# Kernel optimization log

Measured on AMD Instinct MI355X. Metric: run time of the kernel, lower is better.

## Reference

```python
import jax, jax.numpy as jnp
import numpy as np


def _minmax_norm(m):
    # per-sample min-max normalize over all non-batch dims (channel=1, h, w)
    mn = m.min(axis=(1, 2, 3), keepdims=True)
    mx = m.max(axis=(1, 2, 3), keepdims=True)
    return (m - mn) / (mx - mn)


def setup_inputs() -> dict:
    key = jax.random.key(0)
    k1, k2, k3, k4, k5 = jax.random.split(key, 5)
    N, C, H, W = 32, 256, 56, 56
    Ce, He, We = 512, 14, 14
    return {
        "main_inputs": jax.random.normal(k1, (N, C, H, W), dtype=jnp.float32),
        "embedding_inputs": jax.random.normal(k2, (N, Ce, He, We), dtype=jnp.float32),
        "conv_w": jax.random.normal(k3, (C, Ce), dtype=jnp.float32) * (1.0 / np.sqrt(Ce)),
        "conv_b": jax.random.normal(k4, (C,), dtype=jnp.float32) * 0.01,
        "weight": jax.random.normal(k5, (), dtype=jnp.float32),
    }


def reference(main_inputs, embedding_inputs, conv_w, conv_b, weight):
    N, C, H, W = main_inputs.shape
    Ce = embedding_inputs.shape[1]
    # nn.Upsample(size=(H,W), mode='bilinear', align_corners=False) == half-pixel linear resize
    up = jax.image.resize(embedding_inputs, (N, Ce, H, W), method="linear")  # [N,Ce,H,W]
    # 1x1 conv Ce -> C
    emb = jnp.einsum("nchw,oc->nohw", up, conv_w) + conv_b[None, :, None, None]  # [N,C,H,W]
    # reshape_and_normalize_masks(squeeze=True): mean over channels, per-sample min-max
    mask = emb.mean(axis=1, keepdims=True)  # [N,1,H,W]
    mask = _minmax_norm(mask)
    # second call with squeeze=False (inference_x is None): normalize again
    mask = _minmax_norm(mask)
    s = jax.nn.sigmoid(main_inputs)
    return s * mask * weight + s
```

## Files before the change

### kernel.cpp

```cpp
#include <hip/hip_runtime.h>
#include <math.h>

#define W_PART_OFF 0
#define WSUM_OFF   32768
#define P2_OFF     33280
#define MASK_OFF   83456

__global__ void k_wsum_part(const float* __restrict__ conv_w, float* __restrict__ ws) {
    int b = blockIdx.x;
    int t = threadIdx.x;
    float a0 = 0.f, a1 = 0.f;
    int o0 = b * 4;
#pragma unroll
    for (int o = o0; o < o0 + 4; ++o) {
        a0 += conv_w[o * 512 + t];
        a1 += conv_w[o * 512 + t + 256];
    }
    ws[W_PART_OFF + b * 512 + t]       = a0;
    ws[W_PART_OFF + b * 512 + t + 256] = a1;
}

__global__ void k_wsum_final(float* __restrict__ ws) {
    int c = blockIdx.x * 256 + threadIdx.x;
    float a = 0.f;
#pragma unroll 8
    for (int k = 0; k < 64; ++k) a += ws[W_PART_OFF + k * 512 + c];
    ws[WSUM_OFF + c] = a;
}

__global__ void k_mask_small(const float* __restrict__ emb, float* __restrict__ ws) {
    __shared__ float wl[64];
    int n  = blockIdx.x;
    int cc = blockIdx.y;
    int t  = threadIdx.x;
    if (t < 64) wl[t] = ws[WSUM_OFF + cc * 64 + t];
    __syncthreads();
    if (t < 196) {
        const float* base = emb + (size_t)(n * 512 + cc * 64) * 196 + t;
        float acc = 0.f;
#pragma unroll 8
        for (int c = 0; c < 64; ++c) acc += base[c * 196] * wl[c];
        ws[P2_OFF + (n * 8 + cc) * 196 + t] = acc;
    }
}

__global__ void k_upsample(const float* __restrict__ wgt_p, float* __restrict__ ws) {
    __shared__ float sm[196];
    __shared__ float rmin[256], rmax[256];
    int n = blockIdx.x;
    int t = threadIdx.x;

    if (t < 196) {
        float a = 0.f;
#pragma unroll
        for (int k = 0; k < 8; ++k) a += ws[P2_OFF + (n * 8 + k) * 196 + t];
        sm[t] = a;
    }
    __syncthreads();

    float vmin = INFINITY, vmax = -INFINITY;
    for (int p = t; p < 3136; p += 256) {
        int h = p / 56, w = p % 56;
        float sy = (h + 0.5f) * 0.25f - 0.5f;
        float sx = (w + 0.5f) * 0.25f - 0.5f;
        int y0 = (int)floorf(sy); float fy = sy - (float)y0;
        int x0 = (int)floorf(sx); float fx = sx - (float)x0;
        int y1 = min(y0 + 1, 13); y0 = max(y0, 0);
        int x1 = min(x0 + 1, 13); x0 = max(x0, 0);
        float v00 = sm[y0 * 14 + x0], v01 = sm[y0 * 14 + x1];
        float v10 = sm[y1 * 14 + x0], v11 = sm[y1 * 14 + x1];
        float v = (1.f - fy) * ((1.f - fx) * v00 + fx * v01)
                +        fy  * ((1.f - fx) * v10 + fx * v11);
        vmin = fminf(vmin, v);
        vmax = fmaxf(vmax, v);
    }
    rmin[t] = vmin; rmax[t] = vmax;
    __syncthreads();
    for (int s = 128; s > 0; s >>= 1) {
        if (t < s) {
            rmin[t] = fminf(rmin[t], rmin[t + s]);
            rmax[t] = fmaxf(rmax[t], rmax[t + s]);
        }
        __syncthreads();
    }
    float mn = rmin[0], mx = rmax[0];
    float a = wgt_p[0] / (mx - mn);
    float b = 1.f - mn * a;

    for (int p = t; p < 3136; p += 256) {
        int h = p / 56, w = p % 56;
        float sy = (h + 0.5f) * 0.25f - 0.5f;
        float sx = (w + 0.5f) * 0.25f - 0.5f;
        int y0 = (int)floorf(sy); float fy = sy - (float)y0;
        int x0 = (int)floorf(sx); float fx = sx - (float)x0;
        int y1 = min(y0 + 1, 13); y0 = max(y0, 0);
        int x1 = min(x0 + 1, 13); x0 = max(x0, 0);
        float v00 = sm[y0 * 14 + x0], v01 = sm[y0 * 14 + x1];
        float v10 = sm[y1 * 14 + x0], v11 = sm[y1 * 14 + x1];
        float v = (1.f - fy) * ((1.f - fx) * v00 + fx * v01)
                +        fy  * ((1.f - fx) * v10 + fx * v11);
        ws[MASK_OFF + n * 3136 + p] = v * a + b;
    }
}

__global__ void __launch_bounds__(256) k_final(const float4* __restrict__ x4,
                                               const float* __restrict__ ws,
                                               float4* __restrict__ out4) {
    const float4* m4 = (const float4*)(ws + MASK_OFF);
    const int total4 = 6422528;
    int stride = gridDim.x * blockDim.x;
    for (int g = blockIdx.x * blockDim.x + threadIdx.x; g < total4; g += stride) {
        int n  = g / 200704;
        int p4 = g % 784;
        float4 m = m4[n * 784 + p4];
        float4 x = x4[g];
        float4 o;
        o.x = m.x * __builtin_amdgcn_rcpf(1.f + __expf(-x.x));
        o.y = m.y * __builtin_amdgcn_rcpf(1.f + __expf(-x.y));
        o.z = m.z * __builtin_amdgcn_rcpf(1.f + __expf(-x.z));
        o.w = m.w * __builtin_amdgcn_rcpf(1.f + __expf(-x.w));
        out4[g] = o;
    }
}

extern "C" void kernel_launch(void* const* d_in, const int* in_sizes, int n_in,
                              void* d_out, int out_size, void* d_ws, size_t ws_size,
                              hipStream_t stream) {
    const float* main_in = (const float*)d_in[0];
    const float* emb_in  = (const float*)d_in[1];
    const float* conv_w  = (const float*)d_in[2];
    const float* weight  = (const float*)d_in[4];

    float* ws  = (float*)d_ws;
    float4* out = (float4*)d_out;

    k_wsum_part <<<64,            256, 0, stream>>>(conv_w, ws);
    k_wsum_final<<<2,             256, 0, stream>>>(ws);
    k_mask_small<<<dim3(32, 8),   256, 0, stream>>>(emb_in, ws);
    k_upsample  <<<32,            256, 0, stream>>>(weight, ws);
    k_final     <<<2048,          256, 0, stream>>>((const float4*)main_in, ws, out);
}
```

Measured before the change: 56.50 us.

## Restructure final kernel with per-sample LDS mask and nontemporal stores

The final elementwise kernel drops the grid-stride loop for a fixed mapping in which each block handles 4096 float4s of one sample. That sample's mask is staged once in shared memory, and the per-element divide/modulo indexing is replaced by an incrementally wrapped index. Outputs are written with nontemporal stores so the streamed output does not pollute cache. The cost is a shared-memory fill plus a barrier per block, and a grid size hard-coded to the problem shape.

```diff
diff --git a/kernel.cpp b/kernel.cpp
--- a/kernel.cpp
+++ b/kernel.cpp
@@ -1,5 +1,7 @@
 #include <hip/hip_runtime.h>
 #include <math.h>
+
+typedef float vfloat4 __attribute__((ext_vector_type(4)));
 
 #define W_PART_OFF 0
 #define WSUM_OFF   32768
@@ -106,20 +108,32 @@
 __global__ void __launch_bounds__(256) k_final(const float4* __restrict__ x4,
                                                const float* __restrict__ ws,
                                                float4* __restrict__ out4) {
-    const float4* m4 = (const float4*)(ws + MASK_OFF);
-    const int total4 = 6422528;
-    int stride = gridDim.x * blockDim.x;
-    for (int g = blockIdx.x * blockDim.x + threadIdx.x; g < total4; g += stride) {
-        int n  = g / 200704;
-        int p4 = g % 784;
-        float4 m = m4[n * 784 + p4];
-        float4 x = x4[g];
-        float4 o;
+    __shared__ float4 mlds[784];
+    const int bid = blockIdx.x;
+    const int t   = threadIdx.x;
+    const int n   = bid / 49;
+    const int s   = bid - n * 49;
+    const float4* m4 = (const float4*)(ws + MASK_OFF) + n * 784;
+    for (int k = t; k < 784; k += 256) mlds[k] = m4[k];
+    __syncthreads();
+
+    const long base = (long)n * 200704 + (long)s * 4096;
+    const float4* xp = x4 + base;
+    vfloat4*      op = (vfloat4*)(out4 + base);
+    int p = (s * 176 + t) % 784;
+
+#pragma unroll 8
+    for (int i = 0; i < 16; ++i) {
+        float4 x = xp[i * 256 + t];
+        float4 m = mlds[p];
+        vfloat4 o;
         o.x = m.x * __builtin_amdgcn_rcpf(1.f + __expf(-x.x));
         o.y = m.y * __builtin_amdgcn_rcpf(1.f + __expf(-x.y));
         o.z = m.z * __builtin_amdgcn_rcpf(1.f + __expf(-x.z));
         o.w = m.w * __builtin_amdgcn_rcpf(1.f + __expf(-x.w));
-        out4[g] = o;
+        __builtin_nontemporal_store(o, &op[i * 256 + t]);
+        p += 256;
+        if (p >= 784) p -= 784;
     }
 }
 
@@ -131,12 +145,12 @@
     const float* conv_w  = (const float*)d_in[2];
     const float* weight  = (const float*)d_in[4];
 
-    float* ws  = (float*)d_ws;
+    float* ws   = (float*)d_ws;
     float4* out = (float4*)d_out;
 
-    k_wsum_part <<<64,            256, 0, stream>>>(conv_w, ws);
-    k_wsum_final<<<2,             256, 0, stream>>>(ws);
-    k_mask_small<<<dim3(32, 8),   256, 0, stream>>>(emb_in, ws);
-    k_upsample  <<<32,            256, 0, stream>>>(weight, ws);
-    k_final     <<<2048,          256, 0, stream>>>((const float4*)main_in, ws, out);
+    k_wsum_part <<<64,          256, 0, stream>>>(conv_w, ws);
+    k_wsum_final<<<2,           256, 0, stream>>>(ws);
+    k_mask_small<<<dim3(32, 8), 256, 0, stream>>>(emb_in, ws);
+    k_upsample  <<<32,          256, 0, stream>>>(weight, ws);
+    k_final     <<<1568,        256, 0, stream>>>((const float4*)main_in, ws, out);
 }
```

After: 56.95 us. No clear change (+0.8%).

## Fuse weight column-sum into mask kernel and tile final kernel per sample

Applied to the files above, without the earlier changes.

Drops the two weight-sum kernels. Each k_mask_small block now recomputes the 64-channel slice of the conv_w column sums it needs, which removes two launches and their serialization. k_final switches from a grid-stride loop to a 2D grid (196 tiles by 32 samples) where each thread handles four float4s, so the integer div/mod per element goes away. The cost is redundant conv_w reads across the 32 sample blocks, and a fixed 1024-float4 tile that assumes these exact shapes.

```diff
diff --git a/kernel.cpp b/kernel.cpp
--- a/kernel.cpp
+++ b/kernel.cpp
@@ -1,40 +1,28 @@
 #include <hip/hip_runtime.h>
 #include <math.h>
 
-#define W_PART_OFF 0
-#define WSUM_OFF   32768
 #define P2_OFF     33280
 #define MASK_OFF   83456
 
-__global__ void k_wsum_part(const float* __restrict__ conv_w, float* __restrict__ ws) {
-    int b = blockIdx.x;
-    int t = threadIdx.x;
-    float a0 = 0.f, a1 = 0.f;
-    int o0 = b * 4;
-#pragma unroll
-    for (int o = o0; o < o0 + 4; ++o) {
-        a0 += conv_w[o * 512 + t];
-        a1 += conv_w[o * 512 + t + 256];
-    }
-    ws[W_PART_OFF + b * 512 + t]       = a0;
-    ws[W_PART_OFF + b * 512 + t + 256] = a1;
-}
-
-__global__ void k_wsum_final(float* __restrict__ ws) {
-    int c = blockIdx.x * 256 + threadIdx.x;
-    float a = 0.f;
-#pragma unroll 8
-    for (int k = 0; k < 64; ++k) a += ws[W_PART_OFF + k * 512 + c];
-    ws[WSUM_OFF + c] = a;
-}
-
-__global__ void k_mask_small(const float* __restrict__ emb, float* __restrict__ ws) {
+__global__ void k_mask_small(const float* __restrict__ emb,
+                             const float* __restrict__ conv_w,
+                             float* __restrict__ ws) {
+    __shared__ float wpart[256];
     __shared__ float wl[64];
     int n  = blockIdx.x;
     int cc = blockIdx.y;
     int t  = threadIdx.x;
-    if (t < 64) wl[t] = ws[WSUM_OFF + cc * 64 + t];
+
+    int col = t & 63, rg = t >> 6;
+    float a = 0.f;
+    const float* wp = conv_w + (rg * 64) * 512 + cc * 64 + col;
+#pragma unroll 8
+    for (int k = 0; k < 64; ++k) a += wp[k * 512];
+    wpart[t] = a;
     __syncthreads();
+    if (t < 64) wl[t] = wpart[t] + wpart[t + 64] + wpart[t + 128] + wpart[t + 192];
+    __syncthreads();
+
     if (t < 196) {
         const float* base = emb + (size_t)(n * 512 + cc * 64) * 196 + t;
         float acc = 0.f;
@@ -106,20 +94,29 @@
 __global__ void __launch_bounds__(256) k_final(const float4* __restrict__ x4,
                                                const float* __restrict__ ws,
                                                float4* __restrict__ out4) {
-    const float4* m4 = (const float4*)(ws + MASK_OFF);
-    const int total4 = 6422528;
-    int stride = gridDim.x * blockDim.x;
-    for (int g = blockIdx.x * blockDim.x + threadIdx.x; g < total4; g += stride) {
-        int n  = g / 200704;
-        int p4 = g % 784;
-        float4 m = m4[n * 784 + p4];
-        float4 x = x4[g];
+    const int t = threadIdx.x;
+    const int s = blockIdx.x;
+    const int n = blockIdx.y;
+    const float4* m4 = (const float4*)(ws + MASK_OFF) + n * 784;
+
+    const long base = (long)n * 200704 + (long)s * 1024;
+    const float4* xp = x4   + base;
+    float4*       op = out4 + base;
+
+    const int p0 = (s * 240 + t) % 784;
+
+#pragma unroll
+    for (int i = 0; i < 4; ++i) {
+        int q = p0 + i * 256;
+        if (q >= 784) q -= 784;
+        float4 x = xp[i * 256 + t];
+        float4 m = m4[q];
         float4 o;
         o.x = m.x * __builtin_amdgcn_rcpf(1.f + __expf(-x.x));
         o.y = m.y * __builtin_amdgcn_rcpf(1.f + __expf(-x.y));
         o.z = m.z * __builtin_amdgcn_rcpf(1.f + __expf(-x.z));
         o.w = m.w * __builtin_amdgcn_rcpf(1.f + __expf(-x.w));
-        out4[g] = o;
+        op[i * 256 + t] = o;
     }
 }
 
@@ -131,12 +128,10 @@
     const float* conv_w  = (const float*)d_in[2];
     const float* weight  = (const float*)d_in[4];
 
-    float* ws  = (float*)d_ws;
+    float* ws   = (float*)d_ws;
     float4* out = (float4*)d_out;
 
-    k_wsum_part <<<64,            256, 0, stream>>>(conv_w, ws);
-    k_wsum_final<<<2,             256, 0, stream>>>(ws);
-    k_mask_small<<<dim3(32, 8),   256, 0, stream>>>(emb_in, ws);
+    k_mask_small<<<dim3(32, 8),   256, 0, stream>>>(emb_in, conv_w, ws);
     k_upsample  <<<32,            256, 0, stream>>>(weight, ws);
-    k_final     <<<2048,          256, 0, stream>>>((const float4*)main_in, ws, out);
+    k_final     <<<dim3(196, 32), 256, 0, stream>>>((const float4*)main_in, ws, out);
 }
```

Measured after the change: 48.55 us. 1.16x faster.
